# Performance work log

Measured on AMD Instinct MI355X. Metric: run time of the kernel, lower is better.

Reference implementation:

```python
import jax, jax.numpy as jnp
import numpy as np

DIM, HEADS, K = 128, 4, 7
HD = DIM // HEADS


def _nbr_idx(n, k):
    # NATTEN boundary-clamped neighborhood (dilation=1): window start clamped to [0, n-k]
    i = np.arange(n)
    start = np.clip(i - k // 2, 0, n - k)
    idx = start[:, None] + np.arange(k)[None, :]          # (n, k) absolute neighbor index
    rel = idx - i[:, None] + (k - 1)                      # (n, k) index into 2k-1 rpb axis
    return jnp.asarray(idx), jnp.asarray(rel)


def _ln(x, w, b, eps=1e-5):
    mu = jnp.mean(x, -1, keepdims=True)
    var = jnp.var(x, -1, keepdims=True)
    return (x - mu) * jax.lax.rsqrt(var + eps) * w + b


def setup_inputs() -> dict:
    key = jax.random.key(0)
    ks = jax.random.split(key, 16)
    B, H, W, C = 1, 128, 128, DIM
    f = jax.random.normal
    inp = {
        'x': f(ks[0], (B, H, W, C), jnp.float32),
        'y': f(ks[1], (B, H, W, C), jnp.float32),
        'qv_w': f(ks[2], (2 * C, C), jnp.float32) * 0.02,
        'qv_b': jnp.zeros((2 * C,), jnp.float32),
        'k_w': f(ks[3], (C, C), jnp.float32) * 0.02,
        'k_b': jnp.zeros((C,), jnp.float32),
        'rpb': f(ks[4], (HEADS, 2 * K - 1, 2 * K - 1), jnp.float32) * 0.02,
        'proj_w': f(ks[5], (C, C), jnp.float32) * 0.02,
        'proj_b': jnp.zeros((C,), jnp.float32),
        'n1_w': jnp.ones((C,), jnp.float32),
        'n1_b': jnp.zeros((C,), jnp.float32),
        'n2_w': jnp.ones((C,), jnp.float32),
        'n2_b': jnp.zeros((C,), jnp.float32),
        'fc1_w': f(ks[6], (4 * C, C), jnp.float32) * 0.02,
        'fc1_b': jnp.zeros((4 * C,), jnp.float32),
        'fc2_w': f(ks[7], (C, 4 * C), jnp.float32) * 0.02,
        'fc2_b': jnp.zeros((C,), jnp.float32),
    }
    return inp


def _block(x, y, qv_w, qv_b, k_w, k_b, rpb, proj_w, proj_b,
           n1_w, n1_b, n2_w, n2_b, fc1_w, fc1_b, fc2_w, fc2_b):
    B, H, W, C = x.shape
    scale = HD ** -0.5
    # ---- CrossNat2D attention on norm1(x) vs y ----
    xn = _ln(x, n1_w, n1_b)
    qv = xn @ qv_w.T + qv_b                               # (B,H,W,2C)
    q = qv[..., :C].reshape(B, H, W, HEADS, HD) * scale
    v = qv[..., C:].reshape(B, H, W, HEADS, HD)
    k = (y @ k_w.T + k_b).reshape(B, H, W, HEADS, HD)

    idx_h, rel_h = _nbr_idx(H, K)
    idx_w, rel_w = _nbr_idx(W, K)
    # gather neighborhoods: (B, H, K, W, K, HEADS, HD)
    k_nbr = k[:, idx_h][:, :, :, idx_w]
    v_nbr = v[:, idx_h][:, :, :, idx_w]

    # attention logits over KxK neighborhood
    attn = jnp.einsum('bijhd,biajchd->bijhac', q, k_nbr)  # (B,H,W,heads,K,K)
    bias = rpb[:, rel_h][..., rel_w]                      # (heads,H,K,W,K)
    attn = attn + jnp.transpose(bias, (1, 3, 0, 2, 4))    # broadcast over B
    attn = jax.nn.softmax(attn.reshape(B, H, W, HEADS, K * K), axis=-1)
    attn = attn.reshape(B, H, W, HEADS, K, K)

    out = jnp.einsum('bijhac,biajchd->bijhd', attn, v_nbr).reshape(B, H, W, C)
    out = out @ proj_w.T + proj_b

    x = x + out
    # ---- MLP ----
    h = _ln(x, n2_w, n2_b) @ fc1_w.T + fc1_b
    h = jax.nn.gelu(h, approximate=False) @ fc2_w.T + fc2_b
    return x + h


def reference(x, y, qv_w, qv_b, k_w, k_b, rpb, proj_w, proj_b,
              n1_w, n1_b, n2_w, n2_b, fc1_w, fc1_b, fc2_w, fc2_b):
    return _block(x, y, qv_w, qv_b, k_w, k_b, rpb, proj_w, proj_b,
                  n1_w, n1_b, n2_w, n2_b, fc1_w, fc1_b, fc2_w, fc2_b)
```

## Files before the change

kernel.cpp:

```cpp
#include <hip/hip_runtime.h>
#include <hip/hip_bf16.h>


#define N_PIX 16384
#define C 128
#define HEADS 4
#define HD 32
#define HW 128

typedef __hip_bfloat16 bf16;
typedef __attribute__((ext_vector_type(8))) short bf16x8;
typedef __attribute__((ext_vector_type(4))) float f32x4;

__device__ __forceinline__ short f2bs(float f) {
    unsigned int r;
    asm("v_cvt_pk_bf16_f32 %0, %1, %2" : "=v"(r) : "v"(f), "v"(f));
    return (short)(r & 0xffff);
}
__device__ __forceinline__ unsigned int pack2(float a, float b) {
    unsigned int r;
    asm("v_cvt_pk_bf16_f32 %0, %1, %2" : "=v"(r) : "v"(a), "v"(b));
    return r;
}
__device__ __forceinline__ float bs2f(short s) {
    __hip_bfloat16_raw r; r.x = (unsigned short)s;
    return __bfloat162float(__hip_bfloat16(r));
}
__device__ __forceinline__ float gelu_f(float v) {
    const float z2 = v * (2.302236206f + 0.102943322f * v * v);
    return v / (1.f + exp2f(-z2));
}

__global__ __launch_bounds__(256) void k_wconv(
    const float* __restrict__ qv_w, const float* __restrict__ k_w,
    const float* __restrict__ proj_w, const float* __restrict__ fc1_w,
    const float* __restrict__ fc2_w,
    short* __restrict__ wqv, short* __restrict__ wk, short* __restrict__ wproj,
    short* __restrict__ wfc1, short* __restrict__ wfc2) {
    const int i = blockIdx.x * 256 + threadIdx.x;
    if (i < 32768) wqv[i] = f2bs(qv_w[i]);
    if (i < 16384) { wk[i] = f2bs(k_w[i]); wproj[i] = f2bs(proj_w[i]); }
    if (i < 65536) { wfc1[i] = f2bs(fc1_w[i]); wfc2[i] = f2bs(fc2_w[i]); }
}

__global__ __launch_bounds__(512, 4) void k_qkv(
    const float* __restrict__ x, const float* __restrict__ y,
    const short* __restrict__ wqv, const float* __restrict__ qv_b,
    const short* __restrict__ wk, const float* __restrict__ k_b,
    const float* __restrict__ n1_w, const float* __restrict__ n1_b,
    bf16* __restrict__ qb, bf16* __restrict__ vb, bf16* __restrict__ kb) {
    __shared__ short xn[64][136];
    __shared__ short yl[64][136];
    const int t = threadIdx.x;
    const int pix0 = ((blockIdx.x & 7) * 32 + (blockIdx.x >> 3)) * 64;
    {
        const int r = t >> 3, c16 = (t & 7) * 16;
        const size_t gp = (size_t)(pix0 + r) * C + c16;
        float xv[16], yv[16];
        *(float4*)&xv[0]  = *(const float4*)(x + gp);
        *(float4*)&xv[4]  = *(const float4*)(x + gp + 4);
        *(float4*)&xv[8]  = *(const float4*)(x + gp + 8);
        *(float4*)&xv[12] = *(const float4*)(x + gp + 12);
        *(float4*)&yv[0]  = *(const float4*)(y + gp);
        *(float4*)&yv[4]  = *(const float4*)(y + gp + 4);
        *(float4*)&yv[8]  = *(const float4*)(y + gp + 8);
        *(float4*)&yv[12] = *(const float4*)(y + gp + 12);
        float sm = 0.f, sq = 0.f;
#pragma unroll
        for (int i2 = 0; i2 < 16; i2++) { sm += xv[i2]; sq += xv[i2] * xv[i2]; }
#pragma unroll
        for (int msk = 1; msk < 8; msk <<= 1) {
            sm += __shfl_xor(sm, msk, 64); sq += __shfl_xor(sq, msk, 64);
        }
        const float mu = sm * (1.f / 128.f);
        const float ri = rsqrtf(sq * (1.f / 128.f) - mu * mu + 1e-5f);
        float w1[16], b1[16];
        *(float4*)&w1[0]  = *(const float4*)(n1_w + c16);
        *(float4*)&w1[4]  = *(const float4*)(n1_w + c16 + 4);
        *(float4*)&w1[8]  = *(const float4*)(n1_w + c16 + 8);
        *(float4*)&w1[12] = *(const float4*)(n1_w + c16 + 12);
        *(float4*)&b1[0]  = *(const float4*)(n1_b + c16);
        *(float4*)&b1[4]  = *(const float4*)(n1_b + c16 + 4);
        *(float4*)&b1[8]  = *(const float4*)(n1_b + c16 + 8);
        *(float4*)&b1[12] = *(const float4*)(n1_b + c16 + 12);
        uint4 o0, o1, p0, p1;
        o0.x = pack2((xv[0] - mu) * ri * w1[0] + b1[0],   (xv[1] - mu) * ri * w1[1] + b1[1]);
        o0.y = pack2((xv[2] - mu) * ri * w1[2] + b1[2],   (xv[3] - mu) * ri * w1[3] + b1[3]);
        o0.z = pack2((xv[4] - mu) * ri * w1[4] + b1[4],   (xv[5] - mu) * ri * w1[5] + b1[5]);
        o0.w = pack2((xv[6] - mu) * ri * w1[6] + b1[6],   (xv[7] - mu) * ri * w1[7] + b1[7]);
        o1.x = pack2((xv[8] - mu) * ri * w1[8] + b1[8],   (xv[9] - mu) * ri * w1[9] + b1[9]);
        o1.y = pack2((xv[10] - mu) * ri * w1[10] + b1[10], (xv[11] - mu) * ri * w1[11] + b1[11]);
        o1.z = pack2((xv[12] - mu) * ri * w1[12] + b1[12], (xv[13] - mu) * ri * w1[13] + b1[13]);
        o1.w = pack2((xv[14] - mu) * ri * w1[14] + b1[14], (xv[15] - mu) * ri * w1[15] + b1[15]);
        p0.x = pack2(yv[0], yv[1]);   p0.y = pack2(yv[2], yv[3]);
        p0.z = pack2(yv[4], yv[5]);   p0.w = pack2(yv[6], yv[7]);
        p1.x = pack2(yv[8], yv[9]);   p1.y = pack2(yv[10], yv[11]);
        p1.z = pack2(yv[12], yv[13]); p1.w = pack2(yv[14], yv[15]);
        *(uint4*)&xn[r][c16] = o0;
        *(uint4*)&xn[r][c16 + 8] = o1;
        *(uint4*)&yl[r][c16] = p0;
        *(uint4*)&yl[r][c16 + 8] = p1;
    }
    __syncthreads();
    const int wave = t >> 6, lane = t & 63, quad = lane >> 4, l15 = lane & 15;
    const float scale = 0.1767766952966369f;
    {
        bf16x8 aA[4][4];
#pragma unroll
        for (int m = 0; m < 4; m++)
#pragma unroll
            for (int kt = 0; kt < 4; kt++)
                aA[m][kt] = *(const bf16x8*)&xn[m * 16 + l15][kt * 32 + quad * 8];
#pragma unroll
        for (int s = 0; s < 2; s++) {
            const int n = (wave * 2 + s) * 16 + l15;
            bf16x8 w[4];
#pragma unroll
            for (int kt = 0; kt < 4; kt++)
                w[kt] = *(const bf16x8*)&wqv[n * C + kt * 32 + quad * 8];
            f32x4 acc[4];
#pragma unroll
            for (int m = 0; m < 4; m++) acc[m] = (f32x4){0.f, 0.f, 0.f, 0.f};
#pragma unroll
            for (int m = 0; m < 4; m++)
#pragma unroll
                for (int kt = 0; kt < 4; kt++)
                    acc[m] = __builtin_amdgcn_mfma_f32_16x16x32_bf16(aA[m][kt], w[kt], acc[m], 0, 0, 0);
            const float bias = qv_b[n];
            if (wave * 2 + s < 8) {
#pragma unroll
                for (int m = 0; m < 4; m++)
#pragma unroll
                    for (int r = 0; r < 4; r++)
                        qb[(size_t)(pix0 + m * 16 + quad * 4 + r) * C + n] =
                            __float2bfloat16((acc[m][r] + bias) * scale);
            } else {
#pragma unroll
                for (int m = 0; m < 4; m++)
#pragma unroll
                    for (int r = 0; r < 4; r++)
                        vb[(size_t)(pix0 + m * 16 + quad * 4 + r) * C + (n - C)] =
                            __float2bfloat16(acc[m][r] + bias);
            }
        }
    }
    {
        bf16x8 aY[4][4];
#pragma unroll
        for (int m = 0; m < 4; m++)
#pragma unroll
            for (int kt = 0; kt < 4; kt++)
                aY[m][kt] = *(const bf16x8*)&yl[m * 16 + l15][kt * 32 + quad * 8];
        const int n = wave * 16 + l15;
        bf16x8 w[4];
#pragma unroll
        for (int kt = 0; kt < 4; kt++)
            w[kt] = *(const bf16x8*)&wk[n * C + kt * 32 + quad * 8];
        f32x4 acc[4];
#pragma unroll
        for (int m = 0; m < 4; m++) acc[m] = (f32x4){0.f, 0.f, 0.f, 0.f};
#pragma unroll
        for (int m = 0; m < 4; m++)
#pragma unroll
            for (int kt = 0; kt < 4; kt++)
                acc[m] = __builtin_amdgcn_mfma_f32_16x16x32_bf16(aY[m][kt], w[kt], acc[m], 0, 0, 0);
        const float bias = k_b[n];
#pragma unroll
        for (int m = 0; m < 4; m++)
#pragma unroll
            for (int r = 0; r < 4; r++)
                kb[(size_t)(pix0 + m * 16 + quad * 4 + r) * C + n] =
                    __float2bfloat16(acc[m][r] + bias);
    }
}

__global__ __launch_bounds__(512, 2) void k_fam(
    const bf16* __restrict__ qb, const bf16* __restrict__ kb,
    const bf16* __restrict__ vb, const float* __restrict__ rpb,
    const float* __restrict__ x,
    const short* __restrict__ wproj, const float* __restrict__ proj_b,
    const float* __restrict__ n2_w, const float* __restrict__ n2_b,
    const short* __restrict__ wfc1, const float* __restrict__ fc1_b,
    const short* __restrict__ wfc2, const float* __restrict__ fc2_b,
    float* __restrict__ out) {
    __shared__ short SH[67104];
    short* const KU  = SH;
    short* const VU  = SH + 25872;
    short* const Pb  = SH + 51744;
    short* const aoL = SH;
    short* const xnb = SH + 8448;
    short* const hb  = SH + 16896;
    short* const x1b = SH + 51744;
    const int t = threadIdx.x;
    const int wave = t >> 6, lane = t & 63, quad = lane >> 4, l15 = lane & 15;
    const int h = wave & 3, mt = wave >> 2;
    const int p = wave & 1, g = wave >> 1;
    const int tile = (blockIdx.x & 7) * 32 + (blockIdx.x >> 3);
    const int i0 = (tile >> 4) * 8, j0 = (tile & 15) * 8;
    const int rs = min(max(i0 - 3, 0), 114);
    const int cs2 = min(max(j0 - 3, 0), 114);
    const int n_0 = (2 * g) * 16 + l15, n_1 = (2 * g + 1) * 16 + l15;
    bf16x8 aQv[2];
#pragma unroll
    for (int u = 0; u < 2; u++) {
        const int q = mt * 2 + u;
        const int iq = i0 + (q >> 1) * 4, jq = j0 + (q & 1) * 4;
        const int pA = (iq + (l15 >> 2)) * HW + jq + (l15 & 3);
        aQv[u] = *(const bf16x8*)(qb + (size_t)pA * C + h * HD + quad * 8);
    }
    float xres[2][2][4];
#pragma unroll
    for (int u = 0; u < 2; u++) {
        const int qm = 2 * p + u;
        const int ib = i0 + (qm >> 1) * 4 + quad, jb = j0 + (qm & 1) * 4;
#pragma unroll
        for (int r = 0; r < 4; r++) {
            const size_t pp = (size_t)(ib * HW + jb + r) * C;
            xres[u][0][r] = x[pp + n_0];
            xres[u][1][r] = x[pp + n_1];
        }
    }
    {
        const int seg = t & 15, r0 = t >> 4;
        int q14 = (r0 >= 28) ? 2 : (r0 >= 14 ? 1 : 0);
        int m14 = r0 - 14 * q14;
        int r = r0;
#pragma unroll
        for (int it = 0; it < 7; it++) {
            if (r < 196) {
                const size_t gp = (size_t)((rs + q14) * HW + (cs2 + m14)) * C + seg * 8;
                *(uint4*)&KU[r * 132 + seg * 8] = *(const uint4*)(kb + gp);
                *(uint4*)&VU[r * 132 + seg * 8] = *(const uint4*)(vb + gp);
            }
            r += 32; q14 += 2; m14 += 4;
            if (m14 >= 14) { m14 -= 14; q14 += 1; }
        }
    }
    int nrA[7], ncA[7];
    {
        int nr = (l15 >= 10) ? 1 : 0;
        int nc = l15 - ((l15 >= 10) ? 10 : 0);
#pragma unroll
        for (int nt = 0; nt < 7; nt++) {
            nrA[nt] = nr; ncA[nt] = nc;
            nc += 6; nr += 1;
            if (nc >= 10) { nc -= 10; nr += 1; }
        }
    }
    __syncthreads();
    const float* rpbh = rpb + h * 169;
    f32x4 Oacc[2][2];
#pragma unroll
    for (int u = 0; u < 2; u++) {
        Oacc[u][0] = (f32x4){0.f, 0.f, 0.f, 0.f};
        Oacc[u][1] = (f32x4){0.f, 0.f, 0.f, 0.f};
    }
#pragma unroll
    for (int u = 0; u < 2; u++) {
        const int q = mt * 2 + u;
        const int iq = i0 + (q >> 1) * 4, jq = j0 + (q & 1) * 4;
        const int rq = min(max(iq - 3, 0), 118), cq = min(max(jq - 3, 0), 118);
        const int vbase = (rq - rs) * 14 + (cq - cs2);
        f32x4 S[7];
#pragma unroll
        for (int nt = 0; nt < 7; nt++) {
            const int lr = min(vbase + nrA[nt] * 14 + ncA[nt], 195);
            const bf16x8 bK = *(const bf16x8*)&KU[lr * 132 + h * HD + quad * 8];
            f32x4 z = {0.f, 0.f, 0.f, 0.f};
            S[nt] = __builtin_amdgcn_mfma_f32_16x16x32_bf16(aQv[u], bK, z, 0, 0, 0);
        }
        float smx[4];
#pragma unroll
        for (int r = 0; r < 4; r++) {
            const int i = iq + quad, j = jq + r;
            const int shi = min(max(i - 3, 0), 121);
            const int swj = min(max(j - 3, 0), 121);
            float best = -1e30f;
#pragma unroll
            for (int nt = 0; nt < 7; nt++) {
                const int ai = rq + nrA[nt], aj = cq + ncA[nt];
                const bool vnb = (nt < 6) | (l15 < 4);
                const bool valid = vnb & (ai >= shi) & (ai <= shi + 6) & (aj >= swj) & (aj <= swj + 6);
                const int ri = min(max(ai - i + 6, 0), 12);
                const int rj = min(max(aj - j + 6, 0), 12);
                const float v = valid ? (S[nt][r] + rpbh[ri * 13 + rj]) : -1e30f;
                S[nt][r] = v;
                best = fmaxf(best, v);
            }
            for (int msk = 1; msk < 16; msk <<= 1) best = fmaxf(best, __shfl_xor(best, msk, 64));
            float s = 0.f;
#pragma unroll
            for (int nt = 0; nt < 7; nt++) {
                const float e = __expf(S[nt][r] - best);
                S[nt][r] = e;
                s += e;
            }
            for (int msk = 1; msk < 16; msk <<= 1) s += __shfl_xor(s, msk, 64);
            smx[r] = 1.f / s;
        }
#pragma unroll
        for (int r = 0; r < 4; r++) {
            short* prow = &Pb[(wave * 16 + quad * 4 + r) * 120];
#pragma unroll
            for (int nt = 0; nt < 7; nt++)
                prow[nt * 16 + l15] = f2bs(S[nt][r] * smx[r]);
        }
#pragma unroll
        for (int kt = 0; kt < 3; kt++) {
            const bf16x8 aP = *(const bf16x8*)&Pb[(wave * 16 + l15) * 120 + kt * 32 + quad * 8];
            const int kbase = kt * 32 + quad * 8;
            int kr = (kbase * 205) >> 11;
            int kc = kbase - 10 * kr;
            int sidx = vbase + kr * 14 + kc;
            int lvr[8];
#pragma unroll
            for (int jj = 0; jj < 8; jj++) {
                lvr[jj] = sidx;
                kc++; sidx++;
                if (kc >= 10) { kc = 0; sidx += 4; }
            }
#pragma unroll
            for (int nt2 = 0; nt2 < 2; nt2++) {
                const int ch = h * HD + nt2 * 16 + l15;
                bf16x8 bV;
#pragma unroll
                for (int jj = 0; jj < 8; jj++) bV[jj] = VU[lvr[jj] * 132 + ch];
                Oacc[u][nt2] = __builtin_amdgcn_mfma_f32_16x16x32_bf16(aP, bV, Oacc[u][nt2], 0, 0, 0);
            }
        }
        {
            bf16x8 aP = {0, 0, 0, 0, 0, 0, 0, 0};
            if (quad < 2) aP = *(const bf16x8*)&Pb[(wave * 16 + l15) * 120 + 96 + quad * 8];
#pragma unroll
            for (int nt2 = 0; nt2 < 2; nt2++) {
                const int ch = h * HD + nt2 * 16 + l15;
                bf16x8 bV = {0, 0, 0, 0, 0, 0, 0, 0};
                if (quad == 0) {
#pragma unroll
                    for (int jj = 0; jj < 8; jj++) {
                        const int kc3 = (6 + jj > 9) ? 9 : 6 + jj;
                        bV[jj] = VU[(vbase + 126 + kc3) * 132 + ch];
                    }
                }
                Oacc[u][nt2] = __builtin_amdgcn_mfma_f32_16x16x32_bf16(aP, bV, Oacc[u][nt2], 0, 0, 0);
            }
        }
    }
    bf16x8 wp0[4], wp1[4];
#pragma unroll
    for (int kt = 0; kt < 4; kt++) {
        wp0[kt] = *(const bf16x8*)&wproj[n_0 * C + kt * 32 + quad * 8];
        wp1[kt] = *(const bf16x8*)&wproj[n_1 * C + kt * 32 + quad * 8];
    }
    __syncthreads();
#pragma unroll
    for (int u = 0; u < 2; u++) {
        const int q = mt * 2 + u;
#pragma unroll
        for (int r = 0; r < 4; r++) {
            const int m = q * 16 + quad * 4 + r;
            aoL[m * 132 + h * HD + l15] = f2bs(Oacc[u][0][r]);
            aoL[m * 132 + h * HD + 16 + l15] = f2bs(Oacc[u][1][r]);
        }
    }
    __syncthreads();
    float x1f[2][2][4];
    {
        bf16x8 aO[2][4];
#pragma unroll
        for (int u = 0; u < 2; u++)
#pragma unroll
            for (int kt = 0; kt < 4; kt++)
                aO[u][kt] = *(const bf16x8*)&aoL[((2 * p + u) * 16 + l15) * 132 + kt * 32 + quad * 8];
        f32x4 pa[2][2];
        pa[0][0] = (f32x4){0.f, 0.f, 0.f, 0.f}; pa[0][1] = (f32x4){0.f, 0.f, 0.f, 0.f};
        pa[1][0] = (f32x4){0.f, 0.f, 0.f, 0.f}; pa[1][1] = (f32x4){0.f, 0.f, 0.f, 0.f};
#pragma unroll
        for (int kt = 0; kt < 4; kt++) {
            pa[0][0] = __builtin_amdgcn_mfma_f32_16x16x32_bf16(aO[0][kt], wp0[kt], pa[0][0], 0, 0, 0);
            pa[0][1] = __builtin_amdgcn_mfma_f32_16x16x32_bf16(aO[0][kt], wp1[kt], pa[0][1], 0, 0, 0);
            pa[1][0] = __builtin_amdgcn_mfma_f32_16x16x32_bf16(aO[1][kt], wp0[kt], pa[1][0], 0, 0, 0);
            pa[1][1] = __builtin_amdgcn_mfma_f32_16x16x32_bf16(aO[1][kt], wp1[kt], pa[1][1], 0, 0, 0);
        }
        const float b0s = proj_b[n_0], b1s = proj_b[n_1];
#pragma unroll
        for (int u = 0; u < 2; u++) {
#pragma unroll
            for (int r = 0; r < 4; r++) {
                const int m = (2 * p + u) * 16 + quad * 4 + r;
                const float v0 = xres[u][0][r] + pa[u][0][r] + b0s;
                const float v1 = xres[u][1][r] + pa[u][1][r] + b1s;
                x1f[u][0][r] = v0; x1f[u][1][r] = v1;
                x1b[m * 132 + n_0] = f2bs(v0);
                x1b[m * 132 + n_1] = f2bs(v1);
            }
        }
    }
    __syncthreads();
    {
        const int row = t >> 3, c16 = (t & 7) * 16;
        float xv[16];
        {
            const uint4 d0 = *(const uint4*)&x1b[row * 132 + c16];
            const uint4 d1 = *(const uint4*)&x1b[row * 132 + c16 + 8];
            const unsigned int w[8] = {d0.x, d0.y, d0.z, d0.w, d1.x, d1.y, d1.z, d1.w};
#pragma unroll
            for (int i2 = 0; i2 < 8; i2++) {
                xv[2 * i2]     = bs2f((short)(w[i2] & 0xffff));
                xv[2 * i2 + 1] = bs2f((short)(w[i2] >> 16));
            }
        }
        float sm = 0.f, sq = 0.f;
#pragma unroll
        for (int i2 = 0; i2 < 16; i2++) { sm += xv[i2]; sq += xv[i2] * xv[i2]; }
#pragma unroll
        for (int msk = 1; msk < 8; msk <<= 1) {
            sm += __shfl_xor(sm, msk, 64); sq += __shfl_xor(sq, msk, 64);
        }
        const float mu = sm * (1.f / 128.f);
        const float ri = rsqrtf(sq * (1.f / 128.f) - mu * mu + 1e-5f);
        float w2[16], b2[16];
        *(float4*)&w2[0]  = *(const float4*)(n2_w + c16);
        *(float4*)&w2[4]  = *(const float4*)(n2_w + c16 + 4);
        *(float4*)&w2[8]  = *(const float4*)(n2_w + c16 + 8);
        *(float4*)&w2[12] = *(const float4*)(n2_w + c16 + 12);
        *(float4*)&b2[0]  = *(const float4*)(n2_b + c16);
        *(float4*)&b2[4]  = *(const float4*)(n2_b + c16 + 4);
        *(float4*)&b2[8]  = *(const float4*)(n2_b + c16 + 8);
        *(float4*)&b2[12] = *(const float4*)(n2_b + c16 + 12);
        uint4 o0, o1;
        o0.x = pack2((xv[0] - mu) * ri * w2[0] + b2[0],   (xv[1] - mu) * ri * w2[1] + b2[1]);
        o0.y = pack2((xv[2] - mu) * ri * w2[2] + b2[2],   (xv[3] - mu) * ri * w2[3] + b2[3]);
        o0.z = pack2((xv[4] - mu) * ri * w2[4] + b2[4],   (xv[5] - mu) * ri * w2[5] + b2[5]);
        o0.w = pack2((xv[6] - mu) * ri * w2[6] + b2[6],   (xv[7] - mu) * ri * w2[7] + b2[7]);
        o1.x = pack2((xv[8] - mu) * ri * w2[8] + b2[8],   (xv[9] - mu) * ri * w2[9] + b2[9]);
        o1.y = pack2((xv[10] - mu) * ri * w2[10] + b2[10], (xv[11] - mu) * ri * w2[11] + b2[11]);
        o1.z = pack2((xv[12] - mu) * ri * w2[12] + b2[12], (xv[13] - mu) * ri * w2[13] + b2[13]);
        o1.w = pack2((xv[14] - mu) * ri * w2[14] + b2[14], (xv[15] - mu) * ri * w2[15] + b2[15]);
        *(uint4*)&xnb[row * 132 + c16] = o0;
        *(uint4*)&xnb[row * 132 + c16 + 8] = o1;
    }
    __syncthreads();
    {
        bf16x8 aX[2][4];
#pragma unroll
        for (int u = 0; u < 2; u++)
#pragma unroll
            for (int kt = 0; kt < 4; kt++)
                aX[u][kt] = *(const bf16x8*)&xnb[((2 * p + u) * 16 + l15) * 132 + kt * 32 + quad * 8];
#pragma unroll
        for (int a = 0; a < 8; a++) {
            const int n = (g * 8 + a) * 16 + l15;
            f32x4 c0 = {0.f, 0.f, 0.f, 0.f}, c1 = {0.f, 0.f, 0.f, 0.f};
#pragma unroll
            for (int kt = 0; kt < 4; kt++) {
                const bf16x8 bw = *(const bf16x8*)&wfc1[n * C + kt * 32 + quad * 8];
                c0 = __builtin_amdgcn_mfma_f32_16x16x32_bf16(aX[0][kt], bw, c0, 0, 0, 0);
                c1 = __builtin_amdgcn_mfma_f32_16x16x32_bf16(aX[1][kt], bw, c1, 0, 0, 0);
            }
            const float bias = fc1_b[n];
#pragma unroll
            for (int r = 0; r < 4; r++) {
                const int m0 = (2 * p) * 16 + quad * 4 + r;
                hb[m0 * 520 + n] = f2bs(gelu_f(c0[r] + bias));
                hb[(m0 + 16) * 520 + n] = f2bs(gelu_f(c1[r] + bias));
            }
        }
    }
    __syncthreads();
    {
        f32x4 f00 = {0.f, 0.f, 0.f, 0.f}, f01 = {0.f, 0.f, 0.f, 0.f};
        f32x4 f10 = {0.f, 0.f, 0.f, 0.f}, f11 = {0.f, 0.f, 0.f, 0.f};
#pragma unroll
        for (int kt = 0; kt < 16; kt++) {
            const bf16x8 a0 = *(const bf16x8*)&hb[((2 * p) * 16 + l15) * 520 + kt * 32 + quad * 8];
            const bf16x8 a1 = *(const bf16x8*)&hb[((2 * p + 1) * 16 + l15) * 520 + kt * 32 + quad * 8];
            const bf16x8 w0 = *(const bf16x8*)&wfc2[n_0 * 512 + kt * 32 + quad * 8];
            const bf16x8 w1 = *(const bf16x8*)&wfc2[n_1 * 512 + kt * 32 + quad * 8];
            f00 = __builtin_amdgcn_mfma_f32_16x16x32_bf16(a0, w0, f00, 0, 0, 0);
            f01 = __builtin_amdgcn_mfma_f32_16x16x32_bf16(a0, w1, f01, 0, 0, 0);
            f10 = __builtin_amdgcn_mfma_f32_16x16x32_bf16(a1, w0, f10, 0, 0, 0);
            f11 = __builtin_amdgcn_mfma_f32_16x16x32_bf16(a1, w1, f11, 0, 0, 0);
        }
        const float b0s = fc2_b[n_0], b1s = fc2_b[n_1];
#pragma unroll
        for (int u = 0; u < 2; u++) {
            const int qm = 2 * p + u;
            const int ib = i0 + (qm >> 1) * 4 + quad, jb = j0 + (qm & 1) * 4;
#pragma unroll
            for (int r = 0; r < 4; r++) {
                const size_t pp = (size_t)(ib * HW + jb + r) * C;
                const float v0 = (u ? f10[r] : f00[r]) + b0s + x1f[u][0][r];
                const float v1 = (u ? f11[r] : f01[r]) + b1s + x1f[u][1][r];
                out[pp + n_0] = v0;
                out[pp + n_1] = v1;
            }
        }
    }
}

extern "C" void kernel_launch(void* const* d_in, const int* in_sizes, int n_in,
                              void* d_out, int out_size, void* d_ws, size_t ws_size,
                              hipStream_t stream) {
    const float* x      = (const float*)d_in[0];
    const float* y      = (const float*)d_in[1];
    const float* qv_w   = (const float*)d_in[2];
    const float* qv_b   = (const float*)d_in[3];
    const float* k_w    = (const float*)d_in[4];
    const float* k_b    = (const float*)d_in[5];
    const float* rpb    = (const float*)d_in[6];
    const float* proj_w = (const float*)d_in[7];
    const float* proj_b = (const float*)d_in[8];
    const float* n1_w   = (const float*)d_in[9];
    const float* n1_b   = (const float*)d_in[10];
    const float* n2_w   = (const float*)d_in[11];
    const float* n2_b   = (const float*)d_in[12];
    const float* fc1_w  = (const float*)d_in[13];
    const float* fc1_b  = (const float*)d_in[14];
    const float* fc2_w  = (const float*)d_in[15];
    const float* fc2_b  = (const float*)d_in[16];
    float* out = (float*)d_out;

    bf16* qb  = (bf16*)d_ws;
    bf16* vb  = qb + (size_t)N_PIX * C;
    bf16* kb  = vb + (size_t)N_PIX * C;
    short* wqv  = (short*)(kb + (size_t)N_PIX * C);
    short* wk   = wqv + 32768;
    short* wproj= wk + 16384;
    short* wfc1 = wproj + 16384;
    short* wfc2 = wfc1 + 65536;

    k_wconv<<<256, 256, 0, stream>>>(qv_w, k_w, proj_w, fc1_w, fc2_w,
                                     wqv, wk, wproj, wfc1, wfc2);
    k_qkv<<<256, 512, 0, stream>>>(x, y, wqv, qv_b, wk, k_b, n1_w, n1_b,
                                   qb, vb, kb);
    k_fam<<<256, 512, 0, stream>>>(qb, kb, vb, rpb, x, wproj, proj_b, n2_w, n2_b,
                                   wfc1, fc1_b, wfc2, fc2_b, out);
}
```

Before: 146.3 us.

## Fuse three kernels into one persistent kernel with grid barriers

```diff
diff --git a/kernel.cpp b/kernel.cpp
--- a/kernel.cpp
+++ b/kernel.cpp
@@ -31,93 +31,149 @@
     return v / (1.f + exp2f(-z2));
 }
 
-__global__ __launch_bounds__(256) void k_wconv(
-    const float* __restrict__ qv_w, const float* __restrict__ k_w,
-    const float* __restrict__ proj_w, const float* __restrict__ fc1_w,
-    const float* __restrict__ fc2_w,
+__device__ __forceinline__ void gridbar(unsigned* c) {
+    __threadfence();
+    __syncthreads();
+    if (threadIdx.x == 0) {
+        atomicAdd(c, 1u);
+        while (atomicAdd(c, 0u) < 256u) __builtin_amdgcn_s_sleep(8);
+    }
+    __syncthreads();
+    __threadfence();
+}
+
+__global__ __launch_bounds__(512, 2) void k_mega(
+    const float* __restrict__ x, const float* __restrict__ y,
+    const float* __restrict__ qv_w, const float* __restrict__ qv_b,
+    const float* __restrict__ k_w, const float* __restrict__ k_b,
+    const float* __restrict__ rpb,
+    const float* __restrict__ proj_w, const float* __restrict__ proj_b,
+    const float* __restrict__ n1_w, const float* __restrict__ n1_b,
+    const float* __restrict__ n2_w, const float* __restrict__ n2_b,
+    const float* __restrict__ fc1_w, const float* __restrict__ fc1_b,
+    const float* __restrict__ fc2_w, const float* __restrict__ fc2_b,
+    bf16* __restrict__ qb, bf16* __restrict__ vb, bf16* __restrict__ kb,
     short* __restrict__ wqv, short* __restrict__ wk, short* __restrict__ wproj,
-    short* __restrict__ wfc1, short* __restrict__ wfc2) {
-    const int i = blockIdx.x * 256 + threadIdx.x;
-    if (i < 32768) wqv[i] = f2bs(qv_w[i]);
-    if (i < 16384) { wk[i] = f2bs(k_w[i]); wproj[i] = f2bs(proj_w[i]); }
-    if (i < 65536) { wfc1[i] = f2bs(fc1_w[i]); wfc2[i] = f2bs(fc2_w[i]); }
-}
-
-__global__ __launch_bounds__(512, 4) void k_qkv(
-    const float* __restrict__ x, const float* __restrict__ y,
-    const short* __restrict__ wqv, const float* __restrict__ qv_b,
-    const short* __restrict__ wk, const float* __restrict__ k_b,
-    const float* __restrict__ n1_w, const float* __restrict__ n1_b,
-    bf16* __restrict__ qb, bf16* __restrict__ vb, bf16* __restrict__ kb) {
-    __shared__ short xn[64][136];
-    __shared__ short yl[64][136];
+    short* __restrict__ wfc1, short* __restrict__ wfc2,
+    unsigned* __restrict__ bar,
+    float* __restrict__ out) {
+    __shared__ __align__(16) short SH[67104];
     const int t = threadIdx.x;
-    const int pix0 = ((blockIdx.x & 7) * 32 + (blockIdx.x >> 3)) * 64;
-    {
-        const int r = t >> 3, c16 = (t & 7) * 16;
-        const size_t gp = (size_t)(pix0 + r) * C + c16;
-        float xv[16], yv[16];
-        *(float4*)&xv[0]  = *(const float4*)(x + gp);
-        *(float4*)&xv[4]  = *(const float4*)(x + gp + 4);
-        *(float4*)&xv[8]  = *(const float4*)(x + gp + 8);
-        *(float4*)&xv[12] = *(const float4*)(x + gp + 12);
-        *(float4*)&yv[0]  = *(const float4*)(y + gp);
-        *(float4*)&yv[4]  = *(const float4*)(y + gp + 4);
-        *(float4*)&yv[8]  = *(const float4*)(y + gp + 8);
-        *(float4*)&yv[12] = *(const float4*)(y + gp + 12);
-        float sm = 0.f, sq = 0.f;
-#pragma unroll
-        for (int i2 = 0; i2 < 16; i2++) { sm += xv[i2]; sq += xv[i2] * xv[i2]; }
-#pragma unroll
-        for (int msk = 1; msk < 8; msk <<= 1) {
-            sm += __shfl_xor(sm, msk, 64); sq += __shfl_xor(sq, msk, 64);
-        }
-        const float mu = sm * (1.f / 128.f);
-        const float ri = rsqrtf(sq * (1.f / 128.f) - mu * mu + 1e-5f);
-        float w1[16], b1[16];
-        *(float4*)&w1[0]  = *(const float4*)(n1_w + c16);
-        *(float4*)&w1[4]  = *(const float4*)(n1_w + c16 + 4);
-        *(float4*)&w1[8]  = *(const float4*)(n1_w + c16 + 8);
-        *(float4*)&w1[12] = *(const float4*)(n1_w + c16 + 12);
-        *(float4*)&b1[0]  = *(const float4*)(n1_b + c16);
-        *(float4*)&b1[4]  = *(const float4*)(n1_b + c16 + 4);
-        *(float4*)&b1[8]  = *(const float4*)(n1_b + c16 + 8);
-        *(float4*)&b1[12] = *(const float4*)(n1_b + c16 + 12);
-        uint4 o0, o1, p0, p1;
-        o0.x = pack2((xv[0] - mu) * ri * w1[0] + b1[0],   (xv[1] - mu) * ri * w1[1] + b1[1]);
-        o0.y = pack2((xv[2] - mu) * ri * w1[2] + b1[2],   (xv[3] - mu) * ri * w1[3] + b1[3]);
-        o0.z = pack2((xv[4] - mu) * ri * w1[4] + b1[4],   (xv[5] - mu) * ri * w1[5] + b1[5]);
-        o0.w = pack2((xv[6] - mu) * ri * w1[6] + b1[6],   (xv[7] - mu) * ri * w1[7] + b1[7]);
-        o1.x = pack2((xv[8] - mu) * ri * w1[8] + b1[8],   (xv[9] - mu) * ri * w1[9] + b1[9]);
-        o1.y = pack2((xv[10] - mu) * ri * w1[10] + b1[10], (xv[11] - mu) * ri * w1[11] + b1[11]);
-        o1.z = pack2((xv[12] - mu) * ri * w1[12] + b1[12], (xv[13] - mu) * ri * w1[13] + b1[13]);
-        o1.w = pack2((xv[14] - mu) * ri * w1[14] + b1[14], (xv[15] - mu) * ri * w1[15] + b1[15]);
-        p0.x = pack2(yv[0], yv[1]);   p0.y = pack2(yv[2], yv[3]);
-        p0.z = pack2(yv[4], yv[5]);   p0.w = pack2(yv[6], yv[7]);
-        p1.x = pack2(yv[8], yv[9]);   p1.y = pack2(yv[10], yv[11]);
-        p1.z = pack2(yv[12], yv[13]); p1.w = pack2(yv[14], yv[15]);
-        *(uint4*)&xn[r][c16] = o0;
-        *(uint4*)&xn[r][c16 + 8] = o1;
-        *(uint4*)&yl[r][c16] = p0;
-        *(uint4*)&yl[r][c16 + 8] = p1;
-    }
-    __syncthreads();
-    const int wave = t >> 6, lane = t & 63, quad = lane >> 4, l15 = lane & 15;
-    const float scale = 0.1767766952966369f;
-    {
-        bf16x8 aA[4][4];
-#pragma unroll
-        for (int m = 0; m < 4; m++)
+    const int bx = blockIdx.x;
+    {
+        const int gi = bx * 512 + t;
+        if (gi < 32768) wqv[gi] = f2bs(qv_w[gi]);
+        if (gi < 16384) { wk[gi] = f2bs(k_w[gi]); wproj[gi] = f2bs(proj_w[gi]); }
+        if (gi < 65536) { wfc1[gi] = f2bs(fc1_w[gi]); wfc2[gi] = f2bs(fc2_w[gi]); }
+    }
+    gridbar(bar + 0);
+    {
+        short (*xn)[136] = (short(*)[136])SH;
+        short (*yl)[136] = (short(*)[136])(SH + 8704);
+        const int pix0 = ((bx & 7) * 32 + (bx >> 3)) * 64;
+        {
+            const int r = t >> 3, c16 = (t & 7) * 16;
+            const size_t gp = (size_t)(pix0 + r) * C + c16;
+            float xv[16], yv[16];
+            *(float4*)&xv[0]  = *(const float4*)(x + gp);
+            *(float4*)&xv[4]  = *(const float4*)(x + gp + 4);
+            *(float4*)&xv[8]  = *(const float4*)(x + gp + 8);
+            *(float4*)&xv[12] = *(const float4*)(x + gp + 12);
+            *(float4*)&yv[0]  = *(const float4*)(y + gp);
+            *(float4*)&yv[4]  = *(const float4*)(y + gp + 4);
+            *(float4*)&yv[8]  = *(const float4*)(y + gp + 8);
+            *(float4*)&yv[12] = *(const float4*)(y + gp + 12);
+            float sm = 0.f, sq = 0.f;
+#pragma unroll
+            for (int i2 = 0; i2 < 16; i2++) { sm += xv[i2]; sq += xv[i2] * xv[i2]; }
+#pragma unroll
+            for (int msk = 1; msk < 8; msk <<= 1) {
+                sm += __shfl_xor(sm, msk, 64); sq += __shfl_xor(sq, msk, 64);
+            }
+            const float mu = sm * (1.f / 128.f);
+            const float ri = rsqrtf(sq * (1.f / 128.f) - mu * mu + 1e-5f);
+            float w1[16], b1[16];
+            *(float4*)&w1[0]  = *(const float4*)(n1_w + c16);
+            *(float4*)&w1[4]  = *(const float4*)(n1_w + c16 + 4);
+            *(float4*)&w1[8]  = *(const float4*)(n1_w + c16 + 8);
+            *(float4*)&w1[12] = *(const float4*)(n1_w + c16 + 12);
+            *(float4*)&b1[0]  = *(const float4*)(n1_b + c16);
+            *(float4*)&b1[4]  = *(const float4*)(n1_b + c16 + 4);
+            *(float4*)&b1[8]  = *(const float4*)(n1_b + c16 + 8);
+            *(float4*)&b1[12] = *(const float4*)(n1_b + c16 + 12);
+            uint4 o0, o1, p0, p1;
+            o0.x = pack2((xv[0] - mu) * ri * w1[0] + b1[0],   (xv[1] - mu) * ri * w1[1] + b1[1]);
+            o0.y = pack2((xv[2] - mu) * ri * w1[2] + b1[2],   (xv[3] - mu) * ri * w1[3] + b1[3]);
+            o0.z = pack2((xv[4] - mu) * ri * w1[4] + b1[4],   (xv[5] - mu) * ri * w1[5] + b1[5]);
+            o0.w = pack2((xv[6] - mu) * ri * w1[6] + b1[6],   (xv[7] - mu) * ri * w1[7] + b1[7]);
+            o1.x = pack2((xv[8] - mu) * ri * w1[8] + b1[8],   (xv[9] - mu) * ri * w1[9] + b1[9]);
+            o1.y = pack2((xv[10] - mu) * ri * w1[10] + b1[10], (xv[11] - mu) * ri * w1[11] + b1[11]);
+            o1.z = pack2((xv[12] - mu) * ri * w1[12] + b1[12], (xv[13] - mu) * ri * w1[13] + b1[13]);
+            o1.w = pack2((xv[14] - mu) * ri * w1[14] + b1[14], (xv[15] - mu) * ri * w1[15] + b1[15]);
+            p0.x = pack2(yv[0], yv[1]);   p0.y = pack2(yv[2], yv[3]);
+            p0.z = pack2(yv[4], yv[5]);   p0.w = pack2(yv[6], yv[7]);
+            p1.x = pack2(yv[8], yv[9]);   p1.y = pack2(yv[10], yv[11]);
+            p1.z = pack2(yv[12], yv[13]); p1.w = pack2(yv[14], yv[15]);
+            *(uint4*)&xn[r][c16] = o0;
+            *(uint4*)&xn[r][c16 + 8] = o1;
+            *(uint4*)&yl[r][c16] = p0;
+            *(uint4*)&yl[r][c16 + 8] = p1;
+        }
+        __syncthreads();
+        const int wave = t >> 6, lane = t & 63, quad = lane >> 4, l15 = lane & 15;
+        const float scale = 0.1767766952966369f;
+        {
+            bf16x8 aA[4][4];
+#pragma unroll
+            for (int m = 0; m < 4; m++)
+#pragma unroll
+                for (int kt = 0; kt < 4; kt++)
+                    aA[m][kt] = *(const bf16x8*)&xn[m * 16 + l15][kt * 32 + quad * 8];
+#pragma unroll
+            for (int s = 0; s < 2; s++) {
+                const int n = (wave * 2 + s) * 16 + l15;
+                bf16x8 w[4];
+#pragma unroll
+                for (int kt = 0; kt < 4; kt++)
+                    w[kt] = *(const bf16x8*)&wqv[n * C + kt * 32 + quad * 8];
+                f32x4 acc[4];
+#pragma unroll
+                for (int m = 0; m < 4; m++) acc[m] = (f32x4){0.f, 0.f, 0.f, 0.f};
+#pragma unroll
+                for (int m = 0; m < 4; m++)
+#pragma unroll
+                    for (int kt = 0; kt < 4; kt++)
+                        acc[m] = __builtin_amdgcn_mfma_f32_16x16x32_bf16(aA[m][kt], w[kt], acc[m], 0, 0, 0);
+                const float bias = qv_b[n];
+                if (wave * 2 + s < 8) {
+#pragma unroll
+                    for (int m = 0; m < 4; m++)
+#pragma unroll
+                        for (int r = 0; r < 4; r++)
+                            qb[(size_t)(pix0 + m * 16 + quad * 4 + r) * C + n] =
+                                __float2bfloat16((acc[m][r] + bias) * scale);
+                } else {
+#pragma unroll
+                    for (int m = 0; m < 4; m++)
+#pragma unroll
+                        for (int r = 0; r < 4; r++)
+                            vb[(size_t)(pix0 + m * 16 + quad * 4 + r) * C + (n - C)] =
+                                __float2bfloat16(acc[m][r] + bias);
+                }
+            }
+        }
+        {
+            bf16x8 aY[4][4];
+#pragma unroll
+            for (int m = 0; m < 4; m++)
+#pragma unroll
+                for (int kt = 0; kt < 4; kt++)
+                    aY[m][kt] = *(const bf16x8*)&yl[m * 16 + l15][kt * 32 + quad * 8];
+            const int n = wave * 16 + l15;
+            bf16x8 w[4];
 #pragma unroll
             for (int kt = 0; kt < 4; kt++)
-                aA[m][kt] = *(const bf16x8*)&xn[m * 16 + l15][kt * 32 + quad * 8];
-#pragma unroll
-        for (int s = 0; s < 2; s++) {
-            const int n = (wave * 2 + s) * 16 + l15;
-            bf16x8 w[4];
-#pragma unroll
-            for (int kt = 0; kt < 4; kt++)
-                w[kt] = *(const bf16x8*)&wqv[n * C + kt * 32 + quad * 8];
+                w[kt] = *(const bf16x8*)&wk[n * C + kt * 32 + quad * 8];
             f32x4 acc[4];
 #pragma unroll
             for (int m = 0; m < 4; m++) acc[m] = (f32x4){0.f, 0.f, 0.f, 0.f};
@@ -125,65 +181,17 @@
             for (int m = 0; m < 4; m++)
 #pragma unroll
                 for (int kt = 0; kt < 4; kt++)
-                    acc[m] = __builtin_amdgcn_mfma_f32_16x16x32_bf16(aA[m][kt], w[kt], acc[m], 0, 0, 0);
-            const float bias = qv_b[n];
-            if (wave * 2 + s < 8) {
-#pragma unroll
-                for (int m = 0; m < 4; m++)
-#pragma unroll
-                    for (int r = 0; r < 4; r++)
-                        qb[(size_t)(pix0 + m * 16 + quad * 4 + r) * C + n] =
-                            __float2bfloat16((acc[m][r] + bias) * scale);
-            } else {
-#pragma unroll
-                for (int m = 0; m < 4; m++)
-#pragma unroll
-                    for (int r = 0; r < 4; r++)
-                        vb[(size_t)(pix0 + m * 16 + quad * 4 + r) * C + (n - C)] =
-                            __float2bfloat16(acc[m][r] + bias);
-            }
-        }
-    }
-    {
-        bf16x8 aY[4][4];
-#pragma unroll
-        for (int m = 0; m < 4; m++)
-#pragma unroll
-            for (int kt = 0; kt < 4; kt++)
-                aY[m][kt] = *(const bf16x8*)&yl[m * 16 + l15][kt * 32 + quad * 8];
-        const int n = wave * 16 + l15;
-        bf16x8 w[4];
-#pragma unroll
-        for (int kt = 0; kt < 4; kt++)
-            w[kt] = *(const bf16x8*)&wk[n * C + kt * 32 + quad * 8];
-        f32x4 acc[4];
-#pragma unroll
-        for (int m = 0; m < 4; m++) acc[m] = (f32x4){0.f, 0.f, 0.f, 0.f};
-#pragma unroll
-        for (int m = 0; m < 4; m++)
-#pragma unroll
-            for (int kt = 0; kt < 4; kt++)
-                acc[m] = __builtin_amdgcn_mfma_f32_16x16x32_bf16(aY[m][kt], w[kt], acc[m], 0, 0, 0);
-        const float bias = k_b[n];
-#pragma unroll
-        for (int m = 0; m < 4; m++)
-#pragma unroll
-            for (int r = 0; r < 4; r++)
-                kb[(size_t)(pix0 + m * 16 + quad * 4 + r) * C + n] =
-                    __float2bfloat16(acc[m][r] + bias);
-    }
-}
-
-__global__ __launch_bounds__(512, 2) void k_fam(
-    const bf16* __restrict__ qb, const bf16* __restrict__ kb,
-    const bf16* __restrict__ vb, const float* __restrict__ rpb,
-    const float* __restrict__ x,
-    const short* __restrict__ wproj, const float* __restrict__ proj_b,
-    const float* __restrict__ n2_w, const float* __restrict__ n2_b,
-    const short* __restrict__ wfc1, const float* __restrict__ fc1_b,
-    const short* __restrict__ wfc2, const float* __restrict__ fc2_b,
-    float* __restrict__ out) {
-    __shared__ short SH[67104];
+                    acc[m] = __builtin_amdgcn_mfma_f32_16x16x32_bf16(aY[m][kt], w[kt], acc[m], 0, 0, 0);
+            const float bias = k_b[n];
+#pragma unroll
+            for (int m = 0; m < 4; m++)
+#pragma unroll
+                for (int r = 0; r < 4; r++)
+                    kb[(size_t)(pix0 + m * 16 + quad * 4 + r) * C + n] =
+                        __float2bfloat16(acc[m][r] + bias);
+        }
+    }
+    gridbar(bar + 1);
     short* const KU  = SH;
     short* const VU  = SH + 25872;
     short* const Pb  = SH + 51744;
@@ -191,11 +199,10 @@
     short* const xnb = SH + 8448;
     short* const hb  = SH + 16896;
     short* const x1b = SH + 51744;
-    const int t = threadIdx.x;
     const int wave = t >> 6, lane = t & 63, quad = lane >> 4, l15 = lane & 15;
     const int h = wave & 3, mt = wave >> 2;
     const int p = wave & 1, g = wave >> 1;
-    const int tile = (blockIdx.x & 7) * 32 + (blockIdx.x >> 3);
+    const int tile = (bx & 7) * 32 + (bx >> 3);
     const int i0 = (tile >> 4) * 8, j0 = (tile & 15) * 8;
     const int rs = min(max(i0 - 3, 0), 114);
     const int cs2 = min(max(j0 - 3, 0), 114);
@@ -529,11 +536,12 @@
     short* wproj= wk + 16384;
     short* wfc1 = wproj + 16384;
     short* wfc2 = wfc1 + 65536;
-
-    k_wconv<<<256, 256, 0, stream>>>(qv_w, k_w, proj_w, fc1_w, fc2_w,
-                                     wqv, wk, wproj, wfc1, wfc2);
-    k_qkv<<<256, 512, 0, stream>>>(x, y, wqv, qv_b, wk, k_b, n1_w, n1_b,
-                                   qb, vb, kb);
-    k_fam<<<256, 512, 0, stream>>>(qb, kb, vb, rpb, x, wproj, proj_b, n2_w, n2_b,
-                                   wfc1, fc1_b, wfc2, fc2_b, out);
-}
+    unsigned* bar = (unsigned*)(wfc2 + 65536);
+
+    hipMemsetAsync(bar, 0, 8, stream);
+    k_mega<<<256, 512, 0, stream>>>(x, y, qv_w, qv_b, k_w, k_b, rpb,
+                                    proj_w, proj_b, n1_w, n1_b, n2_w, n2_b,
+                                    fc1_w, fc1_b, fc2_w, fc2_b,
+                                    qb, vb, kb, wqv, wk, wproj, wfc1, wfc2,
+                                    bar, out);
+}
```

After: 327.1 us. 2.24x slower.

## Fuse weight conversion into QKV kernel and stage QKV weights in LDS

Applied to the files above, without the earlier changes.

```diff
diff --git a/kernel.cpp b/kernel.cpp
--- a/kernel.cpp
+++ b/kernel.cpp
@@ -31,28 +31,47 @@
     return v / (1.f + exp2f(-z2));
 }
 
-__global__ __launch_bounds__(256) void k_wconv(
-    const float* __restrict__ qv_w, const float* __restrict__ k_w,
+__global__ __launch_bounds__(512, 2) void k_qkv(
+    const float* __restrict__ x, const float* __restrict__ y,
+    const float* __restrict__ qv_w, const float* __restrict__ qv_b,
+    const float* __restrict__ k_w, const float* __restrict__ k_b,
+    const float* __restrict__ n1_w, const float* __restrict__ n1_b,
     const float* __restrict__ proj_w, const float* __restrict__ fc1_w,
     const float* __restrict__ fc2_w,
-    short* __restrict__ wqv, short* __restrict__ wk, short* __restrict__ wproj,
-    short* __restrict__ wfc1, short* __restrict__ wfc2) {
-    const int i = blockIdx.x * 256 + threadIdx.x;
-    if (i < 32768) wqv[i] = f2bs(qv_w[i]);
-    if (i < 16384) { wk[i] = f2bs(k_w[i]); wproj[i] = f2bs(proj_w[i]); }
-    if (i < 65536) { wfc1[i] = f2bs(fc1_w[i]); wfc2[i] = f2bs(fc2_w[i]); }
-}
-
-__global__ __launch_bounds__(512, 4) void k_qkv(
-    const float* __restrict__ x, const float* __restrict__ y,
-    const short* __restrict__ wqv, const float* __restrict__ qv_b,
-    const short* __restrict__ wk, const float* __restrict__ k_b,
-    const float* __restrict__ n1_w, const float* __restrict__ n1_b,
-    bf16* __restrict__ qb, bf16* __restrict__ vb, bf16* __restrict__ kb) {
+    bf16* __restrict__ qb, bf16* __restrict__ vb, bf16* __restrict__ kb,
+    short* __restrict__ wproj, short* __restrict__ wfc1,
+    short* __restrict__ wfc2) {
     __shared__ short xn[64][136];
     __shared__ short yl[64][136];
+    __shared__ short wqvL[256 * 136];
+    __shared__ short wkL[128 * 136];
     const int t = threadIdx.x;
     const int pix0 = ((blockIdx.x & 7) * 32 + (blockIdx.x >> 3)) * 64;
+    {
+        const int gi = blockIdx.x * 512 + t;
+        if (gi < 16384) wproj[gi] = f2bs(proj_w[gi]);
+        if (gi < 65536) { wfc1[gi] = f2bs(fc1_w[gi]); wfc2[gi] = f2bs(fc2_w[gi]); }
+    }
+#pragma unroll
+    for (int it = 0; it < 6; it++) {
+        const int c = t + it * 512;
+        const bool isq = (c < 2048);
+        const int cc = isq ? c : c - 2048;
+        const float* src = (isq ? qv_w : k_w) + (size_t)cc * 16;
+        short* dst = (isq ? wqvL : wkL) + (cc >> 3) * 136 + (cc & 7) * 16;
+        float v[16];
+        *(float4*)&v[0]  = *(const float4*)(src);
+        *(float4*)&v[4]  = *(const float4*)(src + 4);
+        *(float4*)&v[8]  = *(const float4*)(src + 8);
+        *(float4*)&v[12] = *(const float4*)(src + 12);
+        uint4 o0, o1;
+        o0.x = pack2(v[0], v[1]);   o0.y = pack2(v[2], v[3]);
+        o0.z = pack2(v[4], v[5]);   o0.w = pack2(v[6], v[7]);
+        o1.x = pack2(v[8], v[9]);   o1.y = pack2(v[10], v[11]);
+        o1.z = pack2(v[12], v[13]); o1.w = pack2(v[14], v[15]);
+        *(uint4*)dst = o0;
+        *(uint4*)(dst + 8) = o1;
+    }
     {
         const int r = t >> 3, c16 = (t & 7) * 16;
         const size_t gp = (size_t)(pix0 + r) * C + c16;
@@ -117,7 +136,7 @@
             bf16x8 w[4];
 #pragma unroll
             for (int kt = 0; kt < 4; kt++)
-                w[kt] = *(const bf16x8*)&wqv[n * C + kt * 32 + quad * 8];
+                w[kt] = *(const bf16x8*)&wqvL[n * 136 + kt * 32 + quad * 8];
             f32x4 acc[4];
 #pragma unroll
             for (int m = 0; m < 4; m++) acc[m] = (f32x4){0.f, 0.f, 0.f, 0.f};
@@ -155,7 +174,7 @@
         bf16x8 w[4];
 #pragma unroll
         for (int kt = 0; kt < 4; kt++)
-            w[kt] = *(const bf16x8*)&wk[n * C + kt * 32 + quad * 8];
+            w[kt] = *(const bf16x8*)&wkL[n * 136 + kt * 32 + quad * 8];
         f32x4 acc[4];
 #pragma unroll
         for (int m = 0; m < 4; m++) acc[m] = (f32x4){0.f, 0.f, 0.f, 0.f};
@@ -524,16 +543,13 @@
     bf16* qb  = (bf16*)d_ws;
     bf16* vb  = qb + (size_t)N_PIX * C;
     bf16* kb  = vb + (size_t)N_PIX * C;
-    short* wqv  = (short*)(kb + (size_t)N_PIX * C);
-    short* wk   = wqv + 32768;
-    short* wproj= wk + 16384;
+    short* wproj= (short*)(kb + (size_t)N_PIX * C);
     short* wfc1 = wproj + 16384;
     short* wfc2 = wfc1 + 65536;
 
-    k_wconv<<<256, 256, 0, stream>>>(qv_w, k_w, proj_w, fc1_w, fc2_w,
-                                     wqv, wk, wproj, wfc1, wfc2);
-    k_qkv<<<256, 512, 0, stream>>>(x, y, wqv, qv_b, wk, k_b, n1_w, n1_b,
-                                   qb, vb, kb);
+    k_qkv<<<256, 512, 0, stream>>>(x, y, qv_w, qv_b, k_w, k_b, n1_w, n1_b,
+                                   proj_w, fc1_w, fc2_w,
+                                   qb, vb, kb, wproj, wfc1, wfc2);
     k_fam<<<256, 512, 0, stream>>>(qb, kb, vb, rpb, x, wproj, proj_b, n2_w, n2_b,
                                    wfc1, fc1_b, wfc2, fc2_b, out);
 }
```

After: 144.8 us (median of 2 runs). No clear change (-1.1%).
